# Kernel optimization log

Measured on AMD Instinct MI355X. Metric: run time of the kernel, lower is better.

The kernel has to match this reference:

```python
import jax, jax.numpy as jnp
import numpy as np

N, E, IN, HID, G, OUT = 50000, 800000, 9, 128, 256, 10
CLUSTERS, NCO, MCO = 20, 6, 4  # numerator deg 5 (6 coeffs), denominator deg 4
EPS = 1e-5


def _gcn(x, W, b, src, dst):
    # PyG GCNConv: x' = D^-1/2 (A + I) D^-1/2 (x W) + b, with self-loops
    n = x.shape[0]
    h = x @ W  # [N, out]
    ones = jnp.ones(src.shape[0], h.dtype)
    deg = jax.ops.segment_sum(ones, dst, num_segments=n) + 1.0  # + self-loop
    dinv = jax.lax.rsqrt(deg)
    coef = (dinv[src] * dinv[dst])[:, None]
    agg = jax.ops.segment_sum(h[src] * coef, dst, num_segments=n)
    agg = agg + h * (dinv * dinv)[:, None]  # self-loop messages
    return agg + b


def _rational(x, num, den, assign):
    # per-cluster safe Pade rational: P_5(x) / (1 + |Q_4(x)|), coeffs gathered per channel
    a = num[assign]  # [HID, 6]
    q = den[assign]  # [HID, 4]
    P = a[:, 5]
    for i in (4, 3, 2, 1, 0):
        P = P * x + a[:, i]
    Q = q[:, 3]
    for i in (2, 1, 0):
        Q = Q * x + q[:, i]
    Q = Q * x  # Q has no constant term
    return P / (1.0 + jnp.abs(Q))


def _bn(x, g, b):
    m = x.mean(axis=0)
    v = x.var(axis=0)
    return g * (x - m) * jax.lax.rsqrt(v + EPS) + b


def setup_inputs() -> dict:
    key = jax.random.key(0)
    ks = jax.random.split(key, 32)
    d = {}
    d["x"] = jax.random.normal(ks[0], (N, IN), jnp.float32)
    d["edge_index"] = jax.random.randint(ks[1], (2, E), 0, N, jnp.int32)
    d["batch"] = jnp.sort(jax.random.randint(ks[2], (N,), 0, G, jnp.int32))
    dims = [(IN, HID), (HID, HID), (HID, HID), (HID, HID)]
    for i, (di, do) in enumerate(dims):
        d[f"W{i}"] = jax.random.normal(ks[3 + i], (di, do), jnp.float32) / np.sqrt(di)
        d[f"b{i}"] = jnp.zeros((do,), jnp.float32)
        d[f"g{i}"] = jnp.ones((do,), jnp.float32)
        d[f"be{i}"] = jnp.zeros((do,), jnp.float32)
    d["rat_num"] = jax.random.normal(ks[10], (CLUSTERS, NCO), jnp.float32) * 0.3
    d["rat_den"] = jax.random.normal(ks[11], (CLUSTERS, MCO), jnp.float32) * 0.3
    d["cluster_assign"] = (jnp.arange(HID) % CLUSTERS).astype(jnp.int32)
    d["HW1"] = jax.random.normal(ks[12], (HID, HID), jnp.float32) / np.sqrt(HID)
    d["Hb1"] = jnp.zeros((HID,), jnp.float32)
    d["HW2"] = jax.random.normal(ks[13], (HID, HID), jnp.float32) / np.sqrt(HID)
    d["Hb2"] = jnp.zeros((HID,), jnp.float32)
    d["HW3"] = jax.random.normal(ks[14], (HID, OUT), jnp.float32) / np.sqrt(HID)
    d["Hb3"] = jnp.zeros((OUT,), jnp.float32)
    return d


def reference(x, edge_index, batch,
              W0, b0, g0, be0, W1, b1, g1, be1,
              W2, b2, g2, be2, W3, b3, g3, be3,
              rat_num, rat_den, cluster_assign,
              HW1, Hb1, HW2, Hb2, HW3, Hb3):
    src, dst = edge_index[0], edge_index[1]
    h = x
    for W, b, g, be in ((W0, b0, g0, be0), (W1, b1, g1, be1),
                        (W2, b2, g2, be2), (W3, b3, g3, be3)):
        h = _gcn(h, W, b, src, dst)
        h = _rational(h, rat_num, rat_den, cluster_assign)
        h = _bn(h, g, be)
        # Dropout(p=0.1): identity in eval mode
    # global mean pool over graphs
    counts = jax.ops.segment_sum(jnp.ones((h.shape[0],), h.dtype), batch, num_segments=G)
    pooled = jax.ops.segment_sum(h, batch, num_segments=G) / jnp.maximum(counts, 1.0)[:, None]
    # MLP head: (Dropout->Linear->GELU) x2, Dropout->Linear
    z = jax.nn.gelu(pooled @ HW1 + Hb1, approximate=False)
    z = jax.nn.gelu(z @ HW2 + Hb2, approximate=False)
    return z @ HW3 + Hb3
```

## Files before the change

### kernel.cpp

```cpp
#include <hip/hip_runtime.h>
#include <math.h>

#define HID 128
#define GRP 256
#define INF 9
#define OUTF 10

typedef _Float16 half8 __attribute__((ext_vector_type(8)));
typedef __attribute__((ext_vector_type(4))) float f32x4;

__global__ void hist_prepw_kernel(const int* __restrict__ ei, int* __restrict__ cnt, int E,
                                  const float* __restrict__ W1, const float* __restrict__ W2,
                                  const float* __restrict__ W3,
                                  _Float16* __restrict__ Whi, _Float16* __restrict__ Wlo) {
    int e = blockIdx.x * 256 + threadIdx.x;
    if (e < E) atomicAdd(&cnt[ei[E + e]], 1);
    if (blockIdx.x < 192) {
        int l = blockIdx.x >> 6;
        int idx = (blockIdx.x & 63) * 256 + threadIdx.x;
        const float* W = (l == 0) ? W1 : (l == 1) ? W2 : W3;
        int nn = idx >> 7, k = idx & 127;
        float w = W[k * HID + nn];
        _Float16 hi = (_Float16)w;
        _Float16 lo = (_Float16)(w - (float)hi);
        int nt = nn >> 4, l16 = nn & 15;
        int kc = k >> 5, quad = (k >> 3) & 3, j = k & 7;
        size_t off = (size_t)(l + 1) * HID * HID +
                     ((((nt * 4 + kc) * 4 + quad) * 16 + l16) * 8 + j);
        Whi[off] = hi;
        Wlo[off] = lo;
    }
}

__global__ __launch_bounds__(256) void scanA_kernel(const int* __restrict__ cnt,
                                                    int* __restrict__ bsum, int n) {
    int tid = threadIdx.x;
    int base = blockIdx.x * 1024 + tid * 4;
    int s = 0;
    #pragma unroll
    for (int i = 0; i < 4; i++) s += (base + i < n) ? cnt[base + i] : 0;
    #pragma unroll
    for (int off = 32; off > 0; off >>= 1) s += __shfl_down(s, off);
    __shared__ int ws[4];
    if ((tid & 63) == 0) ws[tid >> 6] = s;
    __syncthreads();
    if (tid == 0) bsum[blockIdx.x] = ws[0] + ws[1] + ws[2] + ws[3];
}

__global__ void scanB_kernel(int* __restrict__ bsum, int* __restrict__ row_ptr,
                             int nb, int n) {
    int lane = threadIdx.x;
    int carry = 0;
    for (int base = 0; base < nb; base += 64) {
        int v = (base + lane < nb) ? bsum[base + lane] : 0;
        int ps = v;
        #pragma unroll
        for (int off = 1; off < 64; off <<= 1) {
            int t = __shfl_up(ps, off);
            if (lane >= off) ps += t;
        }
        if (base + lane < nb) bsum[base + lane] = carry + ps - v;
        carry += __shfl(ps, 63);
    }
    if (lane == 0) row_ptr[n] = carry;
}

__global__ __launch_bounds__(256) void scanC_kernel(const int* __restrict__ cnt,
                                                    const int* __restrict__ bsum,
                                                    const int* __restrict__ batch,
                                                    int* __restrict__ row_ptr,
                                                    int* __restrict__ cursor,
                                                    float* __restrict__ dinv,
                                                    int* __restrict__ gstart,
                                                    int* __restrict__ gend, int n) {
    int tid = threadIdx.x;
    int lane = tid & 63, wid = tid >> 6;
    int idx0 = blockIdx.x * 1024 + tid * 4;
    int v[4];
    #pragma unroll
    for (int i = 0; i < 4; i++) v[i] = (idx0 + i < n) ? cnt[idx0 + i] : 0;
    int s = v[0] + v[1] + v[2] + v[3];
    int ps = s;
    #pragma unroll
    for (int off = 1; off < 64; off <<= 1) {
        int t = __shfl_up(ps, off);
        if (lane >= off) ps += t;
    }
    __shared__ int wsum[4];
    if (lane == 63) wsum[wid] = ps;
    __syncthreads();
    int woff = 0;
    #pragma unroll
    for (int i = 0; i < 4; i++) if (i < wid) woff += wsum[i];
    int run = bsum[blockIdx.x] + woff + (ps - s);
    #pragma unroll
    for (int i = 0; i < 4; i++) {
        int idx = idx0 + i;
        if (idx < n) {
            row_ptr[idx] = run;
            cursor[idx] = run;
            dinv[idx] = rsqrtf((float)(v[i] + 1));
            run += v[i];
            int b = batch[idx];
            if (idx == 0 || batch[idx - 1] != b) gstart[b] = idx;
            if (idx == n - 1 || batch[idx + 1] != b) gend[b] = idx + 1;
        }
    }
}

__global__ void fill_kernel(const int* __restrict__ ei, int* __restrict__ cursor,
                            const float* __restrict__ dinv,
                            int2* __restrict__ csr, int E) {
    int e = blockIdx.x * blockDim.x + threadIdx.x;
    if (e >= E) return;
    int s = ei[e], d = ei[E + e];
    int pos = atomicAdd(&cursor[d], 1);
    csr[pos] = make_int2(s, __float_as_int(dinv[s] * dinv[d]));
}

__device__ __forceinline__ float rational_act(float xv, const float* __restrict__ a,
                                              const float* __restrict__ q) {
    float P = a[5];
    P = fmaf(P, xv, a[4]); P = fmaf(P, xv, a[3]); P = fmaf(P, xv, a[2]);
    P = fmaf(P, xv, a[1]); P = fmaf(P, xv, a[0]);
    float Q = q[3];
    Q = fmaf(Q, xv, q[2]); Q = fmaf(Q, xv, q[1]); Q = fmaf(Q, xv, q[0]);
    Q *= xv;
    return P / (1.0f + fabsf(Q));
}

__global__ __launch_bounds__(256) void aggx_kernel(const float* __restrict__ x,
                                                   const int* __restrict__ row_ptr,
                                                   const int2* __restrict__ csr,
                                                   const float* __restrict__ dinv,
                                                   float* __restrict__ aggX,
                                                   float* __restrict__ cagg, int n) {
    int tid = threadIdx.x;
    int node = blockIdx.x * 16 + (tid >> 4);
    int lane = tid & 15;
    if (node >= n) return;
    float di = dinv[node];
    float self = di * di;
    float acc = (lane < INF) ? x[node * INF + lane] * self : 0.0f;
    float cfs = self;
    int beg = row_ptr[node], end = row_ptr[node + 1];
    for (int j = beg; j < end; j++) {
        int2 p = csr[j];
        float cf = __int_as_float(p.y);
        cfs += cf;
        if (lane < INF) acc = fmaf(cf, x[p.x * INF + lane], acc);
    }
    if (lane < INF) aggX[node * INF + lane] = acc;
    if (lane == 0) cagg[node] = cfs;
}

__global__ __launch_bounds__(256) void gemm0_fused_kernel(const float* __restrict__ aggX,
                                                          const float* __restrict__ W0,
                                                          const float* __restrict__ b0,
                                                          const float* __restrict__ rat_num,
                                                          const float* __restrict__ rat_den,
                                                          const int* __restrict__ cl_assign,
                                                          _Float16* __restrict__ act,
                                                          float* __restrict__ stat, int n) {
    __shared__ float Ws[INF * HID];
    __shared__ float s_num[120], s_den[80];
    __shared__ int s_cl[HID];
    __shared__ float s_b[HID];
    __shared__ float s_sum[HID], s_sq[HID];
    int tid = threadIdx.x;
    for (int i = tid; i < INF * HID; i += 256) Ws[i] = W0[i];
    if (tid < 120) s_num[tid] = rat_num[tid];
    if (tid < 80) s_den[tid] = rat_den[tid];
    if (tid < HID) {
        s_cl[tid] = cl_assign[tid];
        s_b[tid] = b0[tid];
        s_sum[tid] = 0.0f; s_sq[tid] = 0.0f;
    }
    __syncthreads();
    int c = tid & 127;
    int half = tid >> 7;
    const float* a = s_num + s_cl[c] * 6;
    const float* q = s_den + s_cl[c] * 4;
    float psum = 0.0f, psq = 0.0f;
    for (int node = blockIdx.x * 2 + half; node < n; node += gridDim.x * 2) {
        float acc = s_b[c];
        #pragma unroll
        for (int k = 0; k < INF; k++) acc = fmaf(aggX[node * INF + k], Ws[k * HID + c], acc);
        float r = rational_act(acc, a, q);
        act[node * HID + c] = (_Float16)r;
        psum += r; psq = fmaf(r, r, psq);
    }
    atomicAdd(&s_sum[c], psum);
    atomicAdd(&s_sq[c], psq);
    __syncthreads();
    if (tid < HID) {
        atomicAdd(&stat[tid], s_sum[tid]);
        atomicAdd(&stat[HID + tid], s_sq[tid]);
    }
}

__global__ __launch_bounds__(256) void layer_fused_kernel(const _Float16* __restrict__ act,
                                                          const int2* __restrict__ csr,
                                                          const int* __restrict__ row_ptr,
                                                          const float* __restrict__ dinv,
                                                          const float* __restrict__ cagg,
                                                          const float* __restrict__ statPrev,
                                                          const float* __restrict__ gPrev,
                                                          const float* __restrict__ bePrev,
                                                          const _Float16* __restrict__ Whi,
                                                          const _Float16* __restrict__ Wlo,
                                                          const float* __restrict__ bias,
                                                          const float* __restrict__ rat_num,
                                                          const float* __restrict__ rat_den,
                                                          const int* __restrict__ cl_assign,
                                                          _Float16* __restrict__ actOut,
                                                          float* __restrict__ statOut, int n) {
    __shared__ _Float16 Alds[64 * 136];
    __shared__ int2 s_pair[16][16];
    __shared__ float s_bnw[HID], s_bnu[HID];
    __shared__ float s_num[120], s_den[80];
    __shared__ int s_cl[HID];
    __shared__ float s_bias[HID];
    __shared__ float s_sum[HID], s_sq[HID];
    int tid = threadIdx.x;
    if (tid < 120) s_num[tid] = rat_num[tid];
    if (tid < 80) s_den[tid] = rat_den[tid];
    if (tid < HID) {
        float inv_n = 1.0f / (float)n;
        float mean = statPrev[tid] * inv_n;
        float var = statPrev[HID + tid] * inv_n - mean * mean;
        float w = gPrev[tid] * rsqrtf(var + 1e-5f);
        s_bnw[tid] = w;
        s_bnu[tid] = bePrev[tid] - mean * w;
        s_cl[tid] = cl_assign[tid];
        s_bias[tid] = bias[tid];
        s_sum[tid] = 0.0f; s_sq[tid] = 0.0f;
    }
    __syncthreads();

    int r0 = blockIdx.x * 64;
    int grp = tid >> 4, glane = tid & 15;
    const half8* act8 = (const half8*)act;

    for (int sub = 0; sub < 4; sub++) {
        int lrow = sub * 16 + grp;
        int node = r0 + lrow;
        half8 o;
        if (node < n) {
            float di = dinv[node];
            float selfc = di * di;
            half8 sv = act8[node * 16 + glane];
            float acc[8];
            #pragma unroll
            for (int t = 0; t < 8; t++) acc[t] = (float)sv[t] * selfc;
            int beg = row_ptr[node], end = row_ptr[node + 1];
            for (int base = beg; base < end; base += 16) {
                int m = end - base; if (m > 16) m = 16;
                if (glane < m) s_pair[grp][glane] = csr[base + glane];
                __builtin_amdgcn_wave_barrier();
                int j = 0;
                for (; j + 4 <= m; j += 4) {
                    int2 p0 = s_pair[grp][j],     p1 = s_pair[grp][j + 1];
                    int2 p2 = s_pair[grp][j + 2], p3 = s_pair[grp][j + 3];
                    half8 v0 = act8[p0.x * 16 + glane];
                    half8 v1 = act8[p1.x * 16 + glane];
                    half8 v2 = act8[p2.x * 16 + glane];
                    half8 v3 = act8[p3.x * 16 + glane];
                    float c0 = __int_as_float(p0.y), c1 = __int_as_float(p1.y);
                    float c2 = __int_as_float(p2.y), c3 = __int_as_float(p3.y);
                    #pragma unroll
                    for (int t = 0; t < 8; t++) {
                        acc[t] = fmaf(c0, (float)v0[t], acc[t]);
                        acc[t] = fmaf(c1, (float)v1[t], acc[t]);
                        acc[t] = fmaf(c2, (float)v2[t], acc[t]);
                        acc[t] = fmaf(c3, (float)v3[t], acc[t]);
                    }
                }
                for (; j < m; j++) {
                    int2 p = s_pair[grp][j];
                    float cf = __int_as_float(p.y);
                    half8 v = act8[p.x * 16 + glane];
                    #pragma unroll
                    for (int t = 0; t < 8; t++) acc[t] = fmaf(cf, (float)v[t], acc[t]);
                }
                __builtin_amdgcn_wave_barrier();
            }
            float cg = cagg[node];
            #pragma unroll
            for (int t = 0; t < 8; t++) {
                int c = glane * 8 + t;
                o[t] = (_Float16)fmaf(s_bnw[c], acc[t], s_bnu[c] * cg);
            }
        } else {
            #pragma unroll
            for (int t = 0; t < 8; t++) o[t] = (_Float16)0.0f;
        }
        *(half8*)&Alds[lrow * 136 + glane * 8] = o;
    }
    __syncthreads();

    int w = tid >> 6, l64 = tid & 63;
    int quad = l64 >> 4, l16 = l64 & 15;
    const half8* Bh8 = (const half8*)Whi;
    const half8* Bl8 = (const half8*)Wlo;
    f32x4 acc[8];
    #pragma unroll
    for (int j = 0; j < 8; j++) acc[j] = (f32x4){0.f, 0.f, 0.f, 0.f};
    int lrowA = w * 16 + l16;
    #pragma unroll
    for (int kc = 0; kc < 4; kc++) {
        half8 a = *(const half8*)&Alds[lrowA * 136 + kc * 32 + quad * 8];
        #pragma unroll
        for (int nt = 0; nt < 8; nt++) {
            half8 bh = Bh8[(nt * 4 + kc) * 64 + l64];
            half8 bl = Bl8[(nt * 4 + kc) * 64 + l64];
            acc[nt] = __builtin_amdgcn_mfma_f32_16x16x32_f16(a, bh, acc[nt], 0, 0, 0);
            acc[nt] = __builtin_amdgcn_mfma_f32_16x16x32_f16(a, bl, acc[nt], 0, 0, 0);
        }
    }

    float ps[8], pq[8];
    #pragma unroll
    for (int nt = 0; nt < 8; nt++) { ps[nt] = 0.0f; pq[nt] = 0.0f; }
    #pragma unroll
    for (int reg = 0; reg < 4; reg++) {
        int row = r0 + w * 16 + quad * 4 + reg;
        if (row < n) {
            #pragma unroll
            for (int nt = 0; nt < 8; nt++) {
                int col = nt * 16 + l16;
                float v = acc[nt][reg] + s_bias[col];
                float r = rational_act(v, s_num + s_cl[col] * 6, s_den + s_cl[col] * 4);
                actOut[row * HID + col] = (_Float16)r;
                ps[nt] += r; pq[nt] = fmaf(r, r, pq[nt]);
            }
        }
    }
    #pragma unroll
    for (int nt = 0; nt < 8; nt++) {
        int col = nt * 16 + l16;
        atomicAdd(&s_sum[col], ps[nt]);
        atomicAdd(&s_sq[col], pq[nt]);
    }
    __syncthreads();
    if (tid < HID) {
        atomicAdd(&statOut[tid], s_sum[tid]);
        atomicAdd(&statOut[HID + tid], s_sq[tid]);
    }
}

__global__ __launch_bounds__(256) void poolmlp_kernel(const _Float16* __restrict__ act,
                                                      const int* __restrict__ gstart,
                                                      const int* __restrict__ gend,
                                                      const float* __restrict__ stat,
                                                      const float* __restrict__ g3,
                                                      const float* __restrict__ be3,
                                                      const float* __restrict__ HW1,
                                                      const float* __restrict__ Hb1,
                                                      const float* __restrict__ HW2,
                                                      const float* __restrict__ Hb2,
                                                      const float* __restrict__ HW3,
                                                      const float* __restrict__ Hb3,
                                                      float* __restrict__ out, int n) {
    __shared__ float red[16][HID];
    __shared__ float s_pool[HID];
    __shared__ float s_z[HID];
    int gi = blockIdx.x;
    int tid = threadIdx.x;
    int rg = tid >> 4, lane = tid & 15;
    int s = gstart[gi], e = gend[gi];
    const half8* act8 = (const half8*)act;
    float a[8];
    #pragma unroll
    for (int t = 0; t < 8; t++) a[t] = 0.0f;
    for (int r = s + rg; r < e; r += 16) {
        half8 v = act8[r * 16 + lane];
        #pragma unroll
        for (int t = 0; t < 8; t++) a[t] += (float)v[t];
    }
    #pragma unroll
    for (int t = 0; t < 8; t++) red[rg][lane * 8 + t] = a[t];
    __syncthreads();
    if (tid < HID) {
        float tot = 0.0f;
        #pragma unroll
        for (int i = 0; i < 16; i++) tot += red[i][tid];
        int cnt = e - s;
        float pooled = 0.0f;
        if (cnt > 0) {
            float inv_n = 1.0f / (float)n;
            float mean = stat[tid] * inv_n;
            float var = stat[HID + tid] * inv_n - mean * mean;
            float w = g3[tid] * rsqrtf(var + 1e-5f);
            float u = be3[tid] - mean * w;
            pooled = fmaf(w, tot / (float)cnt, u);
        }
        s_pool[tid] = pooled;
    }
    __syncthreads();
    if (tid < HID) {
        float acc = Hb1[tid];
        #pragma unroll 8
        for (int k = 0; k < HID; k++) acc = fmaf(s_pool[k], HW1[k * HID + tid], acc);
        s_z[tid] = 0.5f * acc * (1.0f + erff(acc * 0.70710678118654752f));
    }
    __syncthreads();
    if (tid < HID) {
        float acc = Hb2[tid];
        #pragma unroll 8
        for (int k = 0; k < HID; k++) acc = fmaf(s_z[k], HW2[k * HID + tid], acc);
        s_pool[tid] = 0.5f * acc * (1.0f + erff(acc * 0.70710678118654752f));
    }
    __syncthreads();
    if (tid < OUTF) {
        float acc = Hb3[tid];
        #pragma unroll 8
        for (int k = 0; k < HID; k++) acc = fmaf(s_pool[k], HW3[k * OUTF + tid], acc);
        out[gi * OUTF + tid] = acc;
    }
}

extern "C" void kernel_launch(void* const* d_in, const int* in_sizes, int n_in,
                              void* d_out, int out_size, void* d_ws, size_t ws_size,
                              hipStream_t stream) {
    const float* x          = (const float*)d_in[0];
    const int*   edge_index = (const int*)d_in[1];
    const int*   batch      = (const int*)d_in[2];
    const float* W[4]  = {(const float*)d_in[3], (const float*)d_in[7], (const float*)d_in[11], (const float*)d_in[15]};
    const float* bL[4] = {(const float*)d_in[4], (const float*)d_in[8], (const float*)d_in[12], (const float*)d_in[16]};
    const float* gL[4] = {(const float*)d_in[5], (const float*)d_in[9], (const float*)d_in[13], (const float*)d_in[17]};
    const float* beL[4]= {(const float*)d_in[6], (const float*)d_in[10], (const float*)d_in[14], (const float*)d_in[18]};
    const float* rat_num = (const float*)d_in[19];
    const float* rat_den = (const float*)d_in[20];
    const int*   cl_assign = (const int*)d_in[21];
    const float* HW1 = (const float*)d_in[22];
    const float* Hb1 = (const float*)d_in[23];
    const float* HW2 = (const float*)d_in[24];
    const float* Hb2 = (const float*)d_in[25];
    const float* HW3 = (const float*)d_in[26];
    const float* Hb3 = (const float*)d_in[27];
    float* out = (float*)d_out;

    const int N = in_sizes[0] / INF;
    const int E = in_sizes[1] / 2;
    const int NB = (N + 1023) / 1024;

    char* wsb = (char*)d_ws;
    size_t o = 0;
    #define ALIGN16 o = (o + 3) & ~(size_t)3;
    int*   cnt     = (int*)(wsb + o * 4);  o += N; ALIGN16
    int*   gstart  = (int*)(wsb + o * 4);  o += GRP;
    int*   gend    = (int*)(wsb + o * 4);  o += GRP;
    float* bnstat  = (float*)(wsb + o * 4); o += 4 * 256;
    size_t zero_elems = o;
    int*   bsum    = (int*)(wsb + o * 4);  o += ((NB + 63) & ~63); ALIGN16
    int*   cursor  = (int*)(wsb + o * 4);  o += N; ALIGN16
    int*   row_ptr = (int*)(wsb + o * 4);  o += N + 1; ALIGN16
    float* dinv    = (float*)(wsb + o * 4); o += N; ALIGN16
    int2*  csr     = (int2*)(wsb + o * 4);  o += 2 * (size_t)E; ALIGN16
    float* aggX    = (float*)(wsb + o * 4); o += (size_t)N * INF; ALIGN16
    _Float16* WhiAll = (_Float16*)(wsb + o * 4); o += 4 * HID * HID / 2; ALIGN16
    _Float16* WloAll = (_Float16*)(wsb + o * 4); o += 4 * HID * HID / 2; ALIGN16
    _Float16* act_h  = (_Float16*)(wsb + o * 4); o += (size_t)N * HID / 2;
    float* cagg = (float*)cnt;

    hipMemsetAsync(d_ws, 0, zero_elems * 4, stream);

    int eb = (E + 255) / 256;
    hist_prepw_kernel<<<eb, 256, 0, stream>>>(edge_index, cnt, E, W[1], W[2], W[3],
                                              WhiAll, WloAll);
    scanA_kernel<<<NB, 256, 0, stream>>>(cnt, bsum, N);
    scanB_kernel<<<1, 64, 0, stream>>>(bsum, row_ptr, NB, N);
    scanC_kernel<<<NB, 256, 0, stream>>>(cnt, bsum, batch, row_ptr, cursor, dinv,
                                         gstart, gend, N);
    fill_kernel<<<eb, 256, 0, stream>>>(edge_index, cursor, dinv, csr, E);

    aggx_kernel<<<(N + 15) / 16, 256, 0, stream>>>(x, row_ptr, csr, dinv, aggX, cagg, N);
    gemm0_fused_kernel<<<1024, 256, 0, stream>>>(aggX, W[0], bL[0], rat_num, rat_den,
                                                 cl_assign, act_h, bnstat, N);

    int layer_grid = (N + 63) / 64;
    for (int l = 1; l < 4; l++) {
        layer_fused_kernel<<<layer_grid, 256, 0, stream>>>(act_h, csr, row_ptr, dinv, cagg,
                                                           bnstat + (l - 1) * 256,
                                                           gL[l - 1], beL[l - 1],
                                                           WhiAll + (size_t)l * HID * HID,
                                                           WloAll + (size_t)l * HID * HID,
                                                           bL[l], rat_num, rat_den, cl_assign,
                                                           act_h, bnstat + l * 256, N);
    }
    poolmlp_kernel<<<GRP, 256, 0, stream>>>(act_h, gstart, gend, bnstat + 3 * 256,
                                            gL[3], beL[3], HW1, Hb1, HW2, Hb2, HW3, Hb3,
                                            out, N);
}
```

Measured before the change: 514.1 us.

## Halve layer tile, broadcast CSR via shuffles, widen gather batches, ping-pong activations

The fused GCN layer kernel now processes 32 rows per block instead of 64 and declares a higher occupancy target in its launch bounds. Neighbor indices and coefficients are held in registers and broadcast with wave shuffles instead of being staged in LDS, and each row's first CSR chunk is prefetched. Neighbor gathers are issued in batches of eight to keep more loads in flight. The MFMA tile is split so each wave covers half the columns, and the BN statistics are reduced with shuffles before fewer LDS atomics. Activations now alternate between two buffers, which removes the in-place read/write hazard across blocks at the cost of an extra N×128 half buffer.

```diff
diff --git a/kernel.cpp b/kernel.cpp
--- a/kernel.cpp
+++ b/kernel.cpp
@@ -199,7 +199,7 @@
     }
 }
 
-__global__ __launch_bounds__(256) void layer_fused_kernel(const _Float16* __restrict__ act,
+__global__ __launch_bounds__(256, 5) void layer_fused_kernel(const _Float16* __restrict__ act,
                                                           const int2* __restrict__ csr,
                                                           const int* __restrict__ row_ptr,
                                                           const float* __restrict__ dinv,
@@ -215,8 +215,7 @@
                                                           const int* __restrict__ cl_assign,
                                                           _Float16* __restrict__ actOut,
                                                           float* __restrict__ statOut, int n) {
-    __shared__ _Float16 Alds[64 * 136];
-    __shared__ int2 s_pair[16][16];
+    __shared__ _Float16 Alds[32 * 136];
     __shared__ float s_bnw[HID], s_bnu[HID];
     __shared__ float s_num[120], s_den[80];
     __shared__ int s_cl[HID];
@@ -238,14 +237,58 @@
     }
     __syncthreads();
 
-    int r0 = blockIdx.x * 64;
+    int r0 = blockIdx.x * 32;
     int grp = tid >> 4, glane = tid & 15;
+    int grpbase = tid & 48;
     const half8* act8 = (const half8*)act;
 
-    for (int sub = 0; sub < 4; sub++) {
+    int nd[2], beg[2], end[2];
+    int2 p0[2]; float c0[2];
+    #pragma unroll
+    for (int sub = 0; sub < 2; sub++) {
+        int node = r0 + sub * 16 + grp;
+        nd[sub] = node;
+        int b = 0, e = 0;
+        if (node < n) { b = row_ptr[node]; e = row_ptr[node + 1]; }
+        beg[sub] = b; end[sub] = e;
+    }
+    #pragma unroll
+    for (int sub = 0; sub < 2; sub++) {
+        int rem = end[sub] - beg[sub];
+        if (rem > 0) {
+            int m = rem < 16 ? rem : 16;
+            int2 p = csr[beg[sub] + (glane < m ? glane : m - 1)];
+            p0[sub] = p;
+            c0[sub] = (glane < m) ? __int_as_float(p.y) : 0.0f;
+        } else {
+            p0[sub] = make_int2(0, 0); c0[sub] = 0.0f;
+        }
+    }
+
+    #define PROCESS8(off)                                                              \
+        {                                                                              \
+            int srcs[8]; float cfs[8];                                                 \
+            _Pragma("unroll")                                                          \
+            for (int u = 0; u < 8; u++) {                                              \
+                srcs[u] = __shfl(cp.x, grpbase + (off) + u, 64);                       \
+                cfs[u]  = __shfl(cc,   grpbase + (off) + u, 64);                       \
+            }                                                                          \
+            half8 v[8];                                                                \
+            _Pragma("unroll")                                                          \
+            for (int u = 0; u < 8; u++) v[u] = act8[srcs[u] * 16 + glane];             \
+            _Pragma("unroll")                                                          \
+            for (int u = 0; u < 8; u++) {                                              \
+                _Pragma("unroll")                                                      \
+                for (int t = 0; t < 8; t++)                                            \
+                    acc[t] = fmaf(cfs[u], (float)v[u][t], acc[t]);                     \
+            }                                                                          \
+        }
+
+    #pragma unroll
+    for (int sub = 0; sub < 2; sub++) {
         int lrow = sub * 16 + grp;
-        int node = r0 + lrow;
         half8 o;
+        int node = nd[sub];
         if (node < n) {
             float di = dinv[node];
             float selfc = di * di;
@@ -253,37 +296,20 @@
             float acc[8];
             #pragma unroll
             for (int t = 0; t < 8; t++) acc[t] = (float)sv[t] * selfc;
-            int beg = row_ptr[node], end = row_ptr[node + 1];
-            for (int base = beg; base < end; base += 16) {
-                int m = end - base; if (m > 16) m = 16;
-                if (glane < m) s_pair[grp][glane] = csr[base + glane];
-                __builtin_amdgcn_wave_barrier();
-                int j = 0;
-                for (; j + 4 <= m; j += 4) {
-                    int2 p0 = s_pair[grp][j],     p1 = s_pair[grp][j + 1];
-                    int2 p2 = s_pair[grp][j + 2], p3 = s_pair[grp][j + 3];
-                    half8 v0 = act8[p0.x * 16 + glane];
-                    half8 v1 = act8[p1.x * 16 + glane];
-                    half8 v2 = act8[p2.x * 16 + glane];
-                    half8 v3 = act8[p3.x * 16 + glane];
-                    float c0 = __int_as_float(p0.y), c1 = __int_as_float(p1.y);
-                    float c2 = __int_as_float(p2.y), c3 = __int_as_float(p3.y);
-                    #pragma unroll
-                    for (int t = 0; t < 8; t++) {
-                        acc[t] = fmaf(c0, (float)v0[t], acc[t]);
-                        acc[t] = fmaf(c1, (float)v1[t], acc[t]);
-                        acc[t] = fmaf(c2, (float)v2[t], acc[t]);
-                        acc[t] = fmaf(c3, (float)v3[t], acc[t]);
-                    }
+            int base = beg[sub];
+            if (base < end[sub]) {
+                int2 cp = p0[sub]; float cc = c0[sub];
+                for (;;) {
+                    int m = end[sub] - base; if (m > 16) m = 16;
+                    PROCESS8(0)
+                    if (m > 8) PROCESS8(8)
+                    base += 16;
+                    if (base >= end[sub]) break;
+                    int mn = end[sub] - base; if (mn > 16) mn = 16;
+                    int2 p = csr[base + (glane < mn ? glane : mn - 1)];
+                    cp = p;
+                    cc = (glane < mn) ? __int_as_float(p.y) : 0.0f;
                 }
-                for (; j < m; j++) {
-                    int2 p = s_pair[grp][j];
-                    float cf = __int_as_float(p.y);
-                    half8 v = act8[p.x * 16 + glane];
-                    #pragma unroll
-                    for (int t = 0; t < 8; t++) acc[t] = fmaf(cf, (float)v[t], acc[t]);
-                }
-                __builtin_amdgcn_wave_barrier();
             }
             float cg = cagg[node];
             #pragma unroll
@@ -297,50 +323,59 @@
         }
         *(half8*)&Alds[lrow * 136 + glane * 8] = o;
     }
+    #undef PROCESS8
     __syncthreads();
 
     int w = tid >> 6, l64 = tid & 63;
     int quad = l64 >> 4, l16 = l64 & 15;
+    int rt = w & 1, nb = w >> 1;
     const half8* Bh8 = (const half8*)Whi;
     const half8* Bl8 = (const half8*)Wlo;
-    f32x4 acc[8];
-    #pragma unroll
-    for (int j = 0; j < 8; j++) acc[j] = (f32x4){0.f, 0.f, 0.f, 0.f};
-    int lrowA = w * 16 + l16;
+    f32x4 acc[4];
+    #pragma unroll
+    for (int j = 0; j < 4; j++) acc[j] = (f32x4){0.f, 0.f, 0.f, 0.f};
+    int lrowA = rt * 16 + l16;
     #pragma unroll
     for (int kc = 0; kc < 4; kc++) {
         half8 a = *(const half8*)&Alds[lrowA * 136 + kc * 32 + quad * 8];
         #pragma unroll
-        for (int nt = 0; nt < 8; nt++) {
-            half8 bh = Bh8[(nt * 4 + kc) * 64 + l64];
-            half8 bl = Bl8[(nt * 4 + kc) * 64 + l64];
-            acc[nt] = __builtin_amdgcn_mfma_f32_16x16x32_f16(a, bh, acc[nt], 0, 0, 0);
-            acc[nt] = __builtin_amdgcn_mfma_f32_16x16x32_f16(a, bl, acc[nt], 0, 0, 0);
-        }
-    }
-
-    float ps[8], pq[8];
-    #pragma unroll
-    for (int nt = 0; nt < 8; nt++) { ps[nt] = 0.0f; pq[nt] = 0.0f; }
+        for (int j = 0; j < 4; j++) {
+            int ntg = nb * 4 + j;
+            half8 bh = Bh8[(ntg * 4 + kc) * 64 + l64];
+            half8 bl = Bl8[(ntg * 4 + kc) * 64 + l64];
+            acc[j] = __builtin_amdgcn_mfma_f32_16x16x32_f16(a, bh, acc[j], 0, 0, 0);
+            acc[j] = __builtin_amdgcn_mfma_f32_16x16x32_f16(a, bl, acc[j], 0, 0, 0);
+        }
+    }
+
+    float ps[4], pq[4];
+    #pragma unroll
+    for (int j = 0; j < 4; j++) { ps[j] = 0.0f; pq[j] = 0.0f; }
     #pragma unroll
     for (int reg = 0; reg < 4; reg++) {
-        int row = r0 + w * 16 + quad * 4 + reg;
+        int row = r0 + rt * 16 + quad * 4 + reg;
         if (row < n) {
             #pragma unroll
-            for (int nt = 0; nt < 8; nt++) {
-                int col = nt * 16 + l16;
-                float v = acc[nt][reg] + s_bias[col];
+            for (int j = 0; j < 4; j++) {
+                int col = (nb * 4 + j) * 16 + l16;
+                float v = acc[j][reg] + s_bias[col];
                 float r = rational_act(v, s_num + s_cl[col] * 6, s_den + s_cl[col] * 4);
                 actOut[row * HID + col] = (_Float16)r;
-                ps[nt] += r; pq[nt] = fmaf(r, r, pq[nt]);
+                ps[j] += r; pq[j] = fmaf(r, r, pq[j]);
             }
         }
     }
     #pragma unroll
-    for (int nt = 0; nt < 8; nt++) {
-        int col = nt * 16 + l16;
-        atomicAdd(&s_sum[col], ps[nt]);
-        atomicAdd(&s_sq[col], pq[nt]);
+    for (int j = 0; j < 4; j++) {
+        float a2 = ps[j] + __shfl_xor(ps[j], 16, 64);
+        a2 += __shfl_xor(a2, 32, 64);
+        float b2 = pq[j] + __shfl_xor(pq[j], 16, 64);
+        b2 += __shfl_xor(b2, 32, 64);
+        if (quad == 0) {
+            int col = (nb * 4 + j) * 16 + l16;
+            atomicAdd(&s_sum[col], a2);
+            atomicAdd(&s_sq[col], b2);
+        }
     }
     __syncthreads();
     if (tid < HID) {
@@ -461,7 +496,8 @@
     float* aggX    = (float*)(wsb + o * 4); o += (size_t)N * INF; ALIGN16
     _Float16* WhiAll = (_Float16*)(wsb + o * 4); o += 4 * HID * HID / 2; ALIGN16
     _Float16* WloAll = (_Float16*)(wsb + o * 4); o += 4 * HID * HID / 2; ALIGN16
-    _Float16* act_h  = (_Float16*)(wsb + o * 4); o += (size_t)N * HID / 2;
+    _Float16* actA  = (_Float16*)(wsb + o * 4); o += (size_t)N * HID / 2; ALIGN16
+    _Float16* actB  = (_Float16*)(wsb + o * 4); o += (size_t)N * HID / 2;
     float* cagg = (float*)cnt;
 
     hipMemsetAsync(d_ws, 0, zero_elems * 4, stream);
@@ -477,19 +513,22 @@
 
     aggx_kernel<<<(N + 15) / 16, 256, 0, stream>>>(x, row_ptr, csr, dinv, aggX, cagg, N);
     gemm0_fused_kernel<<<1024, 256, 0, stream>>>(aggX, W[0], bL[0], rat_num, rat_den,
-                                                 cl_assign, act_h, bnstat, N);
-
-    int layer_grid = (N + 63) / 64;
+                                                 cl_assign, actA, bnstat, N);
+
+    int layer_grid = (N + 31) / 32;
+    _Float16* ain = actA;
+    _Float16* aout = actB;
     for (int l = 1; l < 4; l++) {
-        layer_fused_kernel<<<layer_grid, 256, 0, stream>>>(act_h, csr, row_ptr, dinv, cagg,
+        layer_fused_kernel<<<layer_grid, 256, 0, stream>>>(ain, csr, row_ptr, dinv, cagg,
                                                            bnstat + (l - 1) * 256,
                                                            gL[l - 1], beL[l - 1],
                                                            WhiAll + (size_t)l * HID * HID,
                                                            WloAll + (size_t)l * HID * HID,
                                                            bL[l], rat_num, rat_den, cl_assign,
-                                                           act_h, bnstat + l * 256, N);
-    }
-    poolmlp_kernel<<<GRP, 256, 0, stream>>>(act_h, gstart, gend, bnstat + 3 * 256,
+                                                           aout, bnstat + l * 256, N);
+        _Float16* t = ain; ain = aout; aout = t;
+    }
+    poolmlp_kernel<<<GRP, 256, 0, stream>>>(ain, gstart, gend, bnstat + 3 * 256,
                                             gL[3], beL[3], HW1, Hb1, HW2, Hb2, HW3, Hb3,
                                             out, N);
 }
```

Measured after the change: 597.6 us. 1.16x slower.
